# Optimization experiments

Hardware: AMD Instinct MI355X
Metric: run time of the kernel (lower is better)

Reference implementation:

```python
import jax, jax.numpy as jnp
import numpy as np

D_MODEL = 1024
N_HEADS = 16
D_K = D_MODEL // N_HEADS
BATCH = 2
SEQ = 2048


def setup_inputs() -> dict:
    key = jax.random.key(0)
    ks = jax.random.split(key, 9)
    s = 1.0 / np.sqrt(D_MODEL)
    x = jax.random.normal(ks[0], (BATCH, SEQ, D_MODEL), dtype=jnp.float32)
    # nn.Linear params: weight [out, in], bias [out]
    w_q = jax.random.uniform(ks[1], (D_MODEL, D_MODEL), jnp.float32, -s, s)
    b_q = jax.random.uniform(ks[2], (D_MODEL,), jnp.float32, -s, s)
    w_k = jax.random.uniform(ks[3], (D_MODEL, D_MODEL), jnp.float32, -s, s)
    b_k = jax.random.uniform(ks[4], (D_MODEL,), jnp.float32, -s, s)
    w_v = jax.random.uniform(ks[5], (D_MODEL, D_MODEL), jnp.float32, -s, s)
    b_v = jax.random.uniform(ks[6], (D_MODEL,), jnp.float32, -s, s)
    w_o = jax.random.uniform(ks[7], (D_MODEL, D_MODEL), jnp.float32, -s, s)
    b_o = jax.random.uniform(ks[8], (D_MODEL,), jnp.float32, -s, s)
    return {"x": x, "w_q": w_q, "b_q": b_q, "w_k": w_k, "b_k": b_k,
            "w_v": w_v, "b_v": b_v, "w_o": w_o, "b_o": b_o}


def reference(x, w_q, b_q, w_k, b_k, w_v, b_v, w_o, b_o):
    B, S, _ = x.shape
    # Linear projections, then split heads: [B, H, S, d_k]
    def proj(w, b):
        y = jnp.einsum('bsd,ed->bse', x, w) + b
        return y.reshape(B, S, N_HEADS, D_K).transpose(0, 2, 1, 3)
    q = proj(w_q, b_q)
    k = proj(w_k, b_k)
    v = proj(w_v, b_v)
    scores = jnp.einsum('bhqd,bhkd->bhqk', q, k) / jnp.sqrt(jnp.float32(D_K))
    attn = jax.nn.softmax(scores, axis=-1)  # dropout is identity in eval mode
    out = jnp.einsum('bhqk,bhkd->bhqd', attn, v)
    out = out.transpose(0, 2, 1, 3).reshape(B, S, D_MODEL)
    out = jnp.einsum('bsd,ed->bse', out, w_o) + b_o
    return out, attn
```

## Files before the change

### kernel.cpp

```cpp
#include <hip/hip_runtime.h>
#include <hip/hip_bf16.h>
#include <stdint.h>


typedef __attribute__((ext_vector_type(4))) float f32x4;
typedef __attribute__((ext_vector_type(8))) short s16x8;
typedef __attribute__((ext_vector_type(4))) unsigned int u32x4;
typedef __attribute__((ext_vector_type(4))) unsigned short u16x4;

#define MFMA(a, b, c) __builtin_amdgcn_mfma_f32_16x16x32_bf16((a), (b), (c), 0, 0, 0)

#if __has_builtin(__builtin_amdgcn_exp2f)
#define EXP2(x) __builtin_amdgcn_exp2f(x)
#else
#define EXP2(x) exp2f(x)
#endif

__device__ __forceinline__ unsigned short f2bf(float f) {
    unsigned int u = __float_as_uint(f);
    unsigned int r = (u + 0x7FFFu + ((u >> 16) & 1u)) >> 16;
    return (unsigned short)r;
}
__device__ __forceinline__ unsigned int cvtpk_bf16(float lo, float hi) {
    unsigned int r;
    asm("v_cvt_pk_bf16_f32 %0, %1, %2" : "=v"(r) : "v"(lo), "v"(hi));
    return r;
}

__global__ void convert_kernel(const float* __restrict__ x,
                               const float* __restrict__ wq, const float* __restrict__ wk,
                               const float* __restrict__ wv, const float* __restrict__ wo,
                               unsigned short* __restrict__ xb, unsigned short* __restrict__ wb) {
    size_t g = (size_t)blockIdx.x * blockDim.x + threadIdx.x;
    size_t i4 = g * 4;
    const float* src;
    unsigned short* dst;
    size_t off;
    if (i4 < 4194304) {
        src = x; dst = xb; off = i4;
    } else {
        size_t j = i4 - 4194304;
        int wsel = (int)(j >> 20);
        off = j & 1048575;
        src = (wsel == 0) ? wq : (wsel == 1) ? wk : (wsel == 2) ? wv : wo;
        dst = wb + ((size_t)wsel << 20);
    }
    float4 v = *(const float4*)(src + off);
    u16x4 o;
    o[0] = f2bf(v.x); o[1] = f2bf(v.y); o[2] = f2bf(v.z); o[3] = f2bf(v.w);
    *(u16x4*)(dst + off) = o;
}

__global__ __launch_bounds__(256, 3) void gemm_kernel(
    const unsigned short* __restrict__ A, const unsigned short* __restrict__ B,
    const float* __restrict__ bias_q, const float* __restrict__ bias_k,
    const float* __restrict__ bias_v, int mode,
    unsigned short* __restrict__ Qs, unsigned short* __restrict__ Kb,
    unsigned short* __restrict__ Vt, float* __restrict__ outp) {
    const int t = threadIdx.x;
    const int lane = t & 63;
    const int wv4 = t >> 6;
    const int wr = wv4 >> 1, wc = wv4 & 1;
    const int rowbase = blockIdx.y * 128;
    const int colbase = blockIdx.x * 128;

    __shared__ __align__(16) unsigned short lA[128 * 64];
    __shared__ __align__(16) unsigned short lB[128 * 64];

    const int crow = lane >> 3;
    const int ccol = (lane & 7) * 8;

    f32x4 acc[4][4];
#pragma unroll
    for (int mi = 0; mi < 4; ++mi)
#pragma unroll
        for (int ni = 0; ni < 4; ++ni)
            acc[mi][ni] = (f32x4){0.f, 0.f, 0.f, 0.f};

    const int l15 = lane & 15;
    const int koff = (lane >> 4) * 8;
    const int ar = wr * 64 + l15;
    const int br = wc * 64 + l15;

    for (int kt = 0; kt < 16; ++kt) {
        const int kbase = kt * 64 + ccol;
#pragma unroll
        for (int i = 0; i < 4; ++i) {
            const int c = wv4 * 4 + i;
            const int r = c * 8 + crow;
            __builtin_amdgcn_global_load_lds(
                (const __attribute__((address_space(1))) void*)(A + (size_t)(rowbase + r) * 1024 + kbase),
                (__attribute__((address_space(3))) void*)&lA[c * 512], 16, 0, 0);
            __builtin_amdgcn_global_load_lds(
                (const __attribute__((address_space(1))) void*)(B + (size_t)(colbase + r) * 1024 + kbase),
                (__attribute__((address_space(3))) void*)&lB[c * 512], 16, 0, 0);
        }
        __syncthreads();
#pragma unroll
        for (int kk = 0; kk < 2; ++kk) {
            s16x8 af[4], bf[4];
#pragma unroll
            for (int mi = 0; mi < 4; ++mi)
                af[mi] = *(const s16x8*)&lA[(ar + mi * 16) * 64 + kk * 32 + koff];
#pragma unroll
            for (int ni = 0; ni < 4; ++ni)
                bf[ni] = *(const s16x8*)&lB[(br + ni * 16) * 64 + kk * 32 + koff];
#pragma unroll
            for (int mi = 0; mi < 4; ++mi)
#pragma unroll
                for (int ni = 0; ni < 4; ++ni)
                    acc[mi][ni] = MFMA(af[mi], bf[ni], acc[mi][ni]);
        }
        __syncthreads();
    }

    if (mode == 1) {
#pragma unroll
        for (int ni = 0; ni < 4; ++ni) {
            int n = colbase + wc * 64 + ni * 16 + l15;
            float bv = bias_q[n];
#pragma unroll
            for (int mi = 0; mi < 4; ++mi) {
#pragma unroll
                for (int reg = 0; reg < 4; ++reg) {
                    int m = rowbase + wr * 64 + mi * 16 + (lane >> 4) * 4 + reg;
                    outp[(size_t)m * 1024 + n] = acc[mi][ni][reg] + bv;
                }
            }
        }
    } else {
        const int proj = colbase >> 10;
        const float* bias = (proj == 0) ? bias_q : (proj == 1) ? bias_k : bias_v;
        const float scale = (proj == 0) ? 0.18033688011112042f : 1.0f;
#pragma unroll
        for (int ni = 0; ni < 4; ++ni) {
            int n = colbase + wc * 64 + ni * 16 + l15;
            int nn = n & 1023;
            int h = nn >> 6, d = nn & 63;
            float bv = bias[nn];
#pragma unroll
            for (int mi = 0; mi < 4; ++mi) {
                int m0 = rowbase + wr * 64 + mi * 16 + (lane >> 4) * 4;
                int b = m0 >> 11, s0 = m0 & 2047;
                if (proj == 2) {
                    u16x4 pk;
#pragma unroll
                    for (int reg = 0; reg < 4; ++reg)
                        pk[reg] = f2bf(acc[mi][ni][reg] + bv);
                    int j0 = s0 & 31;
                    int pg = (j0 >> 2) & 3, pn = (j0 >> 4) & 1;
                    int pcol = (s0 & ~31) | (pg << 3) | (pn << 2);
                    *(u16x4*)&Vt[((size_t)(b * 16 + h) * 64 + d) * 2048 + pcol] = pk;
                } else {
                    unsigned short* dstp = (proj == 0) ? Qs : Kb;
#pragma unroll
                    for (int reg = 0; reg < 4; ++reg)
                        dstp[((size_t)(b * 16 + h) * 2048 + (s0 + reg)) * 64 + d] =
                            f2bf((acc[mi][ni][reg] + bv) * scale);
                }
            }
        }
    }
}

__global__ __launch_bounds__(256, 2) void attn_kernel(
    const unsigned short* __restrict__ Qs, const unsigned short* __restrict__ Kb,
    const unsigned short* __restrict__ Vt, float* __restrict__ attn,
    unsigned short* __restrict__ ctx) {
    const int t = threadIdx.x;
    const int lane = t & 63;
    const int l15 = lane & 15;
    const int g = lane >> 4;
    const int g4 = g * 4, g8 = g * 8;
    const int w = t >> 6;
    const int wr = w >> 1, wc = w & 1;
    const int qt = blockIdx.x;
    const int bh = blockIdx.y;
    const int b = bh >> 4, h = bh & 15;

    const unsigned short* Qh = Qs + (size_t)bh * (2048 * 64);
    const unsigned short* Kh = Kb + (size_t)bh * (2048 * 64);
    const unsigned short* Vh = Vt + (size_t)bh * (64 * 2048);
    float* attn_h = attn + (size_t)bh * (2048 * 2048) + (size_t)(qt * 128) * 2048;

    __shared__ float lred[2][128];
    __shared__ float lO[2][64 * 65];

    s16x8 qf[8];
#pragma unroll
    for (int mi = 0; mi < 4; ++mi)
#pragma unroll
        for (int kk = 0; kk < 2; ++kk)
            qf[mi * 2 + kk] =
                *(const s16x8*)&Qh[(size_t)(qt * 128 + wr * 64 + mi * 16 + l15) * 64 + kk * 32 + g8];

    s16x8 kf0[4], kf1[4], vf0[4], vf1[4];

#define K_LOAD(DST, KT)                                                                     \
    {                                                                                       \
        _Pragma("unroll") for (int ni = 0; ni < 2; ++ni)                                    \
            _Pragma("unroll") for (int kk = 0; kk < 2; ++kk)                                \
                DST[ni * 2 + kk] = *(const s16x8*)&Kh[(size_t)((KT) * 64 + wc * 32 +        \
                                                               ni * 16 + l15) * 64 +        \
                                                      kk * 32 + g8];                        \
    }
#define V_LOAD(DST, KT)                                                                     \
    {                                                                                       \
        _Pragma("unroll") for (int db = 0; db < 4; ++db)                                    \
            DST[db] = *(const s16x8*)&Vh[(size_t)(db * 16 + l15) * 2048 +                   \
                                         (KT) * 64 + wc * 32 + g8];                         \
    }
#define QK_MFMA(KF, SACC)                                                                   \
    {                                                                                       \
        _Pragma("unroll") for (int kk = 0; kk < 2; ++kk)                                    \
            _Pragma("unroll") for (int mi = 0; mi < 4; ++mi)                                \
                _Pragma("unroll") for (int ni = 0; ni < 2; ++ni)                            \
                    SACC[mi][ni] = MFMA(KF[ni * 2 + kk], qf[mi * 2 + kk], SACC[mi][ni]);    \
    }

    float qsum[4] = {0.f, 0.f, 0.f, 0.f};
    K_LOAD(kf0, 0);
#define P1_BODY(KF, KFN, KT)                                                                \
    {                                                                                       \
        f32x4 sacc[4][2];                                                                   \
        _Pragma("unroll") for (int mi = 0; mi < 4; ++mi)                                    \
            _Pragma("unroll") for (int ni = 0; ni < 2; ++ni)                                \
                sacc[mi][ni] = (f32x4){0.f, 0.f, 0.f, 0.f};                                 \
        QK_MFMA(KF, sacc);                                                                  \
        if ((KT) < 31) K_LOAD(KFN, (KT) + 1);                                               \
        _Pragma("unroll") for (int mi = 0; mi < 4; ++mi) {                                  \
            float e = 0.f;                                                                  \
            _Pragma("unroll") for (int ni = 0; ni < 2; ++ni)                                \
                _Pragma("unroll") for (int r = 0; r < 4; ++r)                               \
                    e += EXP2(sacc[mi][ni][r]);                                             \
            qsum[mi] += e;                                                                  \
        }                                                                                   \
    }
    for (int k2 = 0; k2 < 16; ++k2) {
        P1_BODY(kf0, kf1, 2 * k2);
        P1_BODY(kf1, kf0, 2 * k2 + 1);
    }
#pragma unroll
    for (int mi = 0; mi < 4; ++mi) {
        float v = qsum[mi];
        v += __shfl_xor(v, 16);
        v += __shfl_xor(v, 32);
        qsum[mi] = v;
    }
    if (lane < 16) {
#pragma unroll
        for (int mi = 0; mi < 4; ++mi)
            lred[wc][wr * 64 + mi * 16 + lane] = qsum[mi];
    }
    __syncthreads();
    float rl[4];
#pragma unroll
    for (int mi = 0; mi < 4; ++mi) {
        int q = wr * 64 + mi * 16 + l15;
        rl[mi] = 1.0f / (lred[0][q] + lred[1][q]);
    }

    f32x4 oacc[4][4];
#pragma unroll
    for (int mi = 0; mi < 4; ++mi)
#pragma unroll
        for (int db = 0; db < 4; ++db) oacc[mi][db] = (f32x4){0.f, 0.f, 0.f, 0.f};

    K_LOAD(kf0, 0);
    V_LOAD(vf0, 0);
#define P2_BODY(KF, KFN, VF, VFN, KT)                                                       \
    {                                                                                       \
        f32x4 sacc[4][2];                                                                   \
        _Pragma("unroll") for (int mi = 0; mi < 4; ++mi)                                    \
            _Pragma("unroll") for (int ni = 0; ni < 2; ++ni)                                \
                sacc[mi][ni] = (f32x4){0.f, 0.f, 0.f, 0.f};                                 \
        QK_MFMA(KF, sacc);                                                                  \
        if ((KT) < 31) {                                                                    \
            K_LOAD(KFN, (KT) + 1);                                                          \
            V_LOAD(VFN, (KT) + 1);                                                          \
        }                                                                                   \
        s16x8 pf[4];                                                                        \
        _Pragma("unroll") for (int mi = 0; mi < 4; ++mi) {                                  \
            const int q = wr * 64 + mi * 16 + l15;                                          \
            float p[8];                                                                     \
            _Pragma("unroll") for (int ni = 0; ni < 2; ++ni) {                              \
                p[ni * 4 + 0] = EXP2(sacc[mi][ni][0]) * rl[mi];                             \
                p[ni * 4 + 1] = EXP2(sacc[mi][ni][1]) * rl[mi];                             \
                p[ni * 4 + 2] = EXP2(sacc[mi][ni][2]) * rl[mi];                             \
                p[ni * 4 + 3] = EXP2(sacc[mi][ni][3]) * rl[mi];                             \
                float4 pv = {p[ni * 4 + 0], p[ni * 4 + 1], p[ni * 4 + 2], p[ni * 4 + 3]};   \
                *(float4*)&attn_h[(size_t)q * 2048 + (KT) * 64 + wc * 32 + ni * 16 + g4] =  \
                    pv;                                                                     \
            }                                                                               \
            u32x4 pkw;                                                                      \
            pkw[0] = cvtpk_bf16(p[0], p[1]);                                                \
            pkw[1] = cvtpk_bf16(p[2], p[3]);                                                \
            pkw[2] = cvtpk_bf16(p[4], p[5]);                                                \
            pkw[3] = cvtpk_bf16(p[6], p[7]);                                                \
            pf[mi] = *(const s16x8*)&pkw;                                                   \
        }                                                                                   \
        _Pragma("unroll") for (int mi = 0; mi < 4; ++mi)                                    \
            _Pragma("unroll") for (int db = 0; db < 4; ++db)                                \
                oacc[mi][db] = MFMA(pf[mi], VF[db], oacc[mi][db]);                          \
    }
    for (int k2 = 0; k2 < 16; ++k2) {
        P2_BODY(kf0, kf1, vf0, vf1, 2 * k2);
        P2_BODY(kf1, kf0, vf1, vf0, 2 * k2 + 1);
    }

    if (wc == 1) {
#pragma unroll
        for (int mi = 0; mi < 4; ++mi)
#pragma unroll
            for (int db = 0; db < 4; ++db)
#pragma unroll
                for (int r = 0; r < 4; ++r)
                    lO[wr][(mi * 16 + g4 + r) * 65 + db * 16 + l15] = oacc[mi][db][r];
    }
    __syncthreads();
    if (wc == 0) {
#pragma unroll
        for (int mi = 0; mi < 4; ++mi) {
#pragma unroll
            for (int db = 0; db < 4; ++db) {
#pragma unroll
                for (int r = 0; r < 4; ++r) {
                    float s = oacc[mi][db][r] + lO[wr][(mi * 16 + g4 + r) * 65 + db * 16 + l15];
                    int q = qt * 128 + wr * 64 + mi * 16 + g4 + r;
                    ctx[((size_t)(b * 2048 + q)) * 1024 + h * 64 + db * 16 + l15] = f2bf(s);
                }
            }
        }
    }
#undef K_LOAD
#undef V_LOAD
#undef QK_MFMA
#undef P1_BODY
#undef P2_BODY
}

extern "C" void kernel_launch(void* const* d_in, const int* in_sizes, int n_in,
                              void* d_out, int out_size, void* d_ws, size_t ws_size,
                              hipStream_t stream) {
    const float* x  = (const float*)d_in[0];
    const float* wq = (const float*)d_in[1];
    const float* bq = (const float*)d_in[2];
    const float* wk = (const float*)d_in[3];
    const float* bk = (const float*)d_in[4];
    const float* wv = (const float*)d_in[5];
    const float* bv = (const float*)d_in[6];
    const float* wo = (const float*)d_in[7];
    const float* bo = (const float*)d_in[8];

    char* ws = (char*)d_ws;
    unsigned short* xb  = (unsigned short*)(ws);
    unsigned short* wb  = (unsigned short*)(ws + 8388608);
    unsigned short* Qsc = (unsigned short*)(ws + 16777216);
    unsigned short* Kb  = (unsigned short*)(ws + 25165824);
    unsigned short* Vt  = (unsigned short*)(ws + 33554432);
    unsigned short* ctx = (unsigned short*)(ws + 41943040);

    float* out  = (float*)d_out;
    float* attn = out + 4194304;

    convert_kernel<<<8192, 256, 0, stream>>>(x, wq, wk, wv, wo, xb, wb);
    gemm_kernel<<<dim3(24, 32), 256, 0, stream>>>(xb, wb, bq, bk, bv, 0,
                                                  Qsc, Kb, Vt, nullptr);
    attn_kernel<<<dim3(16, 32), 256, 0, stream>>>(Qsc, Kb, Vt, attn, ctx);
    gemm_kernel<<<dim3(8, 32), 256, 0, stream>>>(ctx, wb + 3 * 1048576, bo, bo, bo, 1,
                                                 nullptr, nullptr, nullptr, out);
}
```

Before: 276.6 us.

## Restructure attention kernel to one 16-row query strip per wave, 512 threads

The attention kernel now uses 512-thread blocks where each of 8 waves owns 16 query rows across all 64 key columns of a tile. This removes the cross-wave LDS reductions for the softmax denominator and the output accumulator, along with both __syncthreads. A swizzled 1D block index spreads work across XCDs. The explicit double-buffered K/V register prefetch is dropped in favour of plain loads inside each iteration. Each wave now reloads the full K/V tiles, so per-block global/L2 traffic rises and latency hiding depends on occupancy.

```diff
diff --git a/kernel.cpp b/kernel.cpp
--- a/kernel.cpp
+++ b/kernel.cpp
@@ -6,6 +6,7 @@
 typedef __attribute__((ext_vector_type(4))) float f32x4;
 typedef __attribute__((ext_vector_type(8))) short s16x8;
 typedef __attribute__((ext_vector_type(4))) unsigned int u32x4;
+typedef __attribute__((ext_vector_type(2))) unsigned int u32x2;
 typedef __attribute__((ext_vector_type(4))) unsigned short u16x4;
 
 #define MFMA(a, b, c) __builtin_amdgcn_mfma_f32_16x16x32_bf16((a), (b), (c), 0, 0, 0)
@@ -163,7 +164,7 @@
     }
 }
 
-__global__ __launch_bounds__(256, 2) void attn_kernel(
+__global__ __launch_bounds__(512, 4) void attn_kernel(
     const unsigned short* __restrict__ Qs, const unsigned short* __restrict__ Kb,
     const unsigned short* __restrict__ Vt, float* __restrict__ attn,
     unsigned short* __restrict__ ctx) {
@@ -173,170 +174,113 @@
     const int g = lane >> 4;
     const int g4 = g * 4, g8 = g * 8;
     const int w = t >> 6;
-    const int wr = w >> 1, wc = w & 1;
-    const int qt = blockIdx.x;
-    const int bh = blockIdx.y;
+
+    const int wid = (blockIdx.x & 7) * 64 + (blockIdx.x >> 3);
+    const int bh = wid >> 4;
+    const int qt = wid & 15;
     const int b = bh >> 4, h = bh & 15;
 
     const unsigned short* Qh = Qs + (size_t)bh * (2048 * 64);
     const unsigned short* Kh = Kb + (size_t)bh * (2048 * 64);
     const unsigned short* Vh = Vt + (size_t)bh * (64 * 2048);
-    float* attn_h = attn + (size_t)bh * (2048 * 2048) + (size_t)(qt * 128) * 2048;
-
-    __shared__ float lred[2][128];
-    __shared__ float lO[2][64 * 65];
-
-    s16x8 qf[8];
-#pragma unroll
-    for (int mi = 0; mi < 4; ++mi)
+    float* attn_h = attn + (size_t)bh * (2048 * 2048);
+
+    const int qrow = qt * 128 + w * 16;
+
+    s16x8 qf[2];
+#pragma unroll
+    for (int kk = 0; kk < 2; ++kk)
+        qf[kk] = *(const s16x8*)&Qh[(size_t)(qrow + l15) * 64 + kk * 32 + g8];
+
+    float qsum = 0.f;
+    for (int kt = 0; kt < 32; ++kt) {
+        s16x8 kf[8];
+#pragma unroll
+        for (int ni = 0; ni < 4; ++ni)
+#pragma unroll
+            for (int kk = 0; kk < 2; ++kk)
+                kf[ni * 2 + kk] =
+                    *(const s16x8*)&Kh[(size_t)(kt * 64 + ni * 16 + l15) * 64 + kk * 32 + g8];
+        f32x4 sacc[4];
+#pragma unroll
+        for (int ni = 0; ni < 4; ++ni) sacc[ni] = (f32x4){0.f, 0.f, 0.f, 0.f};
 #pragma unroll
         for (int kk = 0; kk < 2; ++kk)
-            qf[mi * 2 + kk] =
-                *(const s16x8*)&Qh[(size_t)(qt * 128 + wr * 64 + mi * 16 + l15) * 64 + kk * 32 + g8];
-
-    s16x8 kf0[4], kf1[4], vf0[4], vf1[4];
-
-#define K_LOAD(DST, KT)                                                                     \
-    {                                                                                       \
-        _Pragma("unroll") for (int ni = 0; ni < 2; ++ni)                                    \
-            _Pragma("unroll") for (int kk = 0; kk < 2; ++kk)                                \
-                DST[ni * 2 + kk] = *(const s16x8*)&Kh[(size_t)((KT) * 64 + wc * 32 +        \
-                                                               ni * 16 + l15) * 64 +        \
-                                                      kk * 32 + g8];                        \
-    }
-#define V_LOAD(DST, KT)                                                                     \
-    {                                                                                       \
-        _Pragma("unroll") for (int db = 0; db < 4; ++db)                                    \
-            DST[db] = *(const s16x8*)&Vh[(size_t)(db * 16 + l15) * 2048 +                   \
-                                         (KT) * 64 + wc * 32 + g8];                         \
-    }
-#define QK_MFMA(KF, SACC)                                                                   \
-    {                                                                                       \
-        _Pragma("unroll") for (int kk = 0; kk < 2; ++kk)                                    \
-            _Pragma("unroll") for (int mi = 0; mi < 4; ++mi)                                \
-                _Pragma("unroll") for (int ni = 0; ni < 2; ++ni)                            \
-                    SACC[mi][ni] = MFMA(KF[ni * 2 + kk], qf[mi * 2 + kk], SACC[mi][ni]);    \
-    }
-
-    float qsum[4] = {0.f, 0.f, 0.f, 0.f};
-    K_LOAD(kf0, 0);
-#define P1_BODY(KF, KFN, KT)                                                                \
-    {                                                                                       \
-        f32x4 sacc[4][2];                                                                   \
-        _Pragma("unroll") for (int mi = 0; mi < 4; ++mi)                                    \
-            _Pragma("unroll") for (int ni = 0; ni < 2; ++ni)                                \
-                sacc[mi][ni] = (f32x4){0.f, 0.f, 0.f, 0.f};                                 \
-        QK_MFMA(KF, sacc);                                                                  \
-        if ((KT) < 31) K_LOAD(KFN, (KT) + 1);                                               \
-        _Pragma("unroll") for (int mi = 0; mi < 4; ++mi) {                                  \
-            float e = 0.f;                                                                  \
-            _Pragma("unroll") for (int ni = 0; ni < 2; ++ni)                                \
-                _Pragma("unroll") for (int r = 0; r < 4; ++r)                               \
-                    e += EXP2(sacc[mi][ni][r]);                                             \
-            qsum[mi] += e;                                                                  \
-        }                                                                                   \
-    }
-    for (int k2 = 0; k2 < 16; ++k2) {
-        P1_BODY(kf0, kf1, 2 * k2);
-        P1_BODY(kf1, kf0, 2 * k2 + 1);
-    }
-#pragma unroll
-    for (int mi = 0; mi < 4; ++mi) {
-        float v = qsum[mi];
-        v += __shfl_xor(v, 16);
-        v += __shfl_xor(v, 32);
-        qsum[mi] = v;
-    }
-    if (lane < 16) {
-#pragma unroll
-        for (int mi = 0; mi < 4; ++mi)
-            lred[wc][wr * 64 + mi * 16 + lane] = qsum[mi];
-    }
-    __syncthreads();
-    float rl[4];
-#pragma unroll
-    for (int mi = 0; mi < 4; ++mi) {
-        int q = wr * 64 + mi * 16 + l15;
-        rl[mi] = 1.0f / (lred[0][q] + lred[1][q]);
-    }
-
-    f32x4 oacc[4][4];
-#pragma unroll
-    for (int mi = 0; mi < 4; ++mi)
-#pragma unroll
-        for (int db = 0; db < 4; ++db) oacc[mi][db] = (f32x4){0.f, 0.f, 0.f, 0.f};
-
-    K_LOAD(kf0, 0);
-    V_LOAD(vf0, 0);
-#define P2_BODY(KF, KFN, VF, VFN, KT)                                                       \
-    {                                                                                       \
-        f32x4 sacc[4][2];                                                                   \
-        _Pragma("unroll") for (int mi = 0; mi < 4; ++mi)                                    \
-            _Pragma("unroll") for (int ni = 0; ni < 2; ++ni)                                \
-                sacc[mi][ni] = (f32x4){0.f, 0.f, 0.f, 0.f};                                 \
-        QK_MFMA(KF, sacc);                                                                  \
-        if ((KT) < 31) {                                                                    \
-            K_LOAD(KFN, (KT) + 1);                                                          \
-            V_LOAD(VFN, (KT) + 1);                                                          \
-        }                                                                                   \
-        s16x8 pf[4];                                                                        \
-        _Pragma("unroll") for (int mi = 0; mi < 4; ++mi) {                                  \
-            const int q = wr * 64 + mi * 16 + l15;                                          \
-            float p[8];                                                                     \
-            _Pragma("unroll") for (int ni = 0; ni < 2; ++ni) {                              \
-                p[ni * 4 + 0] = EXP2(sacc[mi][ni][0]) * rl[mi];                             \
-                p[ni * 4 + 1] = EXP2(sacc[mi][ni][1]) * rl[mi];                             \
-                p[ni * 4 + 2] = EXP2(sacc[mi][ni][2]) * rl[mi];                             \
-                p[ni * 4 + 3] = EXP2(sacc[mi][ni][3]) * rl[mi];                             \
-                float4 pv = {p[ni * 4 + 0], p[ni * 4 + 1], p[ni * 4 + 2], p[ni * 4 + 3]};   \
-                *(float4*)&attn_h[(size_t)q * 2048 + (KT) * 64 + wc * 32 + ni * 16 + g4] =  \
-                    pv;                                                                     \
-            }                                                                               \
-            u32x4 pkw;                                                                      \
-            pkw[0] = cvtpk_bf16(p[0], p[1]);                                                \
-            pkw[1] = cvtpk_bf16(p[2], p[3]);                                                \
-            pkw[2] = cvtpk_bf16(p[4], p[5]);                                                \
-            pkw[3] = cvtpk_bf16(p[6], p[7]);                                                \
-            pf[mi] = *(const s16x8*)&pkw;                                                   \
-        }                                                                                   \
-        _Pragma("unroll") for (int mi = 0; mi < 4; ++mi)                                    \
-            _Pragma("unroll") for (int db = 0; db < 4; ++db)                                \
-                oacc[mi][db] = MFMA(pf[mi], VF[db], oacc[mi][db]);                          \
-    }
-    for (int k2 = 0; k2 < 16; ++k2) {
-        P2_BODY(kf0, kf1, vf0, vf1, 2 * k2);
-        P2_BODY(kf1, kf0, vf1, vf0, 2 * k2 + 1);
-    }
-
-    if (wc == 1) {
-#pragma unroll
-        for (int mi = 0; mi < 4; ++mi)
-#pragma unroll
-            for (int db = 0; db < 4; ++db)
-#pragma unroll
-                for (int r = 0; r < 4; ++r)
-                    lO[wr][(mi * 16 + g4 + r) * 65 + db * 16 + l15] = oacc[mi][db][r];
-    }
-    __syncthreads();
-    if (wc == 0) {
-#pragma unroll
-        for (int mi = 0; mi < 4; ++mi) {
-#pragma unroll
-            for (int db = 0; db < 4; ++db) {
-#pragma unroll
-                for (int r = 0; r < 4; ++r) {
-                    float s = oacc[mi][db][r] + lO[wr][(mi * 16 + g4 + r) * 65 + db * 16 + l15];
-                    int q = qt * 128 + wr * 64 + mi * 16 + g4 + r;
-                    ctx[((size_t)(b * 2048 + q)) * 1024 + h * 64 + db * 16 + l15] = f2bf(s);
-                }
+#pragma unroll
+            for (int ni = 0; ni < 4; ++ni)
+                sacc[ni] = MFMA(kf[ni * 2 + kk], qf[kk], sacc[ni]);
+#pragma unroll
+        for (int ni = 0; ni < 4; ++ni)
+#pragma unroll
+            for (int r = 0; r < 4; ++r) qsum += EXP2(sacc[ni][r]);
+    }
+    qsum += __shfl_xor(qsum, 16);
+    qsum += __shfl_xor(qsum, 32);
+    const float rl = 1.0f / qsum;
+
+    f32x4 oacc[4];
+#pragma unroll
+    for (int db = 0; db < 4; ++db) oacc[db] = (f32x4){0.f, 0.f, 0.f, 0.f};
+
+    for (int kt = 0; kt < 32; ++kt) {
+        s16x8 kf[8];
+#pragma unroll
+        for (int ni = 0; ni < 4; ++ni)
+#pragma unroll
+            for (int kk = 0; kk < 2; ++kk)
+                kf[ni * 2 + kk] =
+                    *(const s16x8*)&Kh[(size_t)(kt * 64 + ni * 16 + l15) * 64 + kk * 32 + g8];
+        s16x8 vf[8];
+#pragma unroll
+        for (int db = 0; db < 4; ++db)
+#pragma unroll
+            for (int ks = 0; ks < 2; ++ks)
+                vf[db * 2 + ks] =
+                    *(const s16x8*)&Vh[(size_t)(db * 16 + l15) * 2048 + kt * 64 + ks * 32 + g8];
+        f32x4 sacc[4];
+#pragma unroll
+        for (int ni = 0; ni < 4; ++ni) sacc[ni] = (f32x4){0.f, 0.f, 0.f, 0.f};
+#pragma unroll
+        for (int kk = 0; kk < 2; ++kk)
+#pragma unroll
+            for (int ni = 0; ni < 4; ++ni)
+                sacc[ni] = MFMA(kf[ni * 2 + kk], qf[kk], sacc[ni]);
+
+        s16x8 pf[2];
+        const int q = qrow + l15;
+#pragma unroll
+        for (int ks = 0; ks < 2; ++ks) {
+            u32x2 w0, w1;
+#pragma unroll
+            for (int nn = 0; nn < 2; ++nn) {
+                const int ni = ks * 2 + nn;
+                float p0 = EXP2(sacc[ni][0]) * rl;
+                float p1 = EXP2(sacc[ni][1]) * rl;
+                float p2 = EXP2(sacc[ni][2]) * rl;
+                float p3 = EXP2(sacc[ni][3]) * rl;
+                f32x4 pv = {p0, p1, p2, p3};
+                *(f32x4*)&attn_h[(size_t)q * 2048 + kt * 64 + ni * 16 + g4] = pv;
+                if (nn == 0) { w0[0] = cvtpk_bf16(p0, p1); w0[1] = cvtpk_bf16(p2, p3); }
+                else         { w1[0] = cvtpk_bf16(p0, p1); w1[1] = cvtpk_bf16(p2, p3); }
             }
-        }
-    }
-#undef K_LOAD
-#undef V_LOAD
-#undef QK_MFMA
-#undef P1_BODY
-#undef P2_BODY
+            u32x4 pkw = {w0[0], w0[1], w1[0], w1[1]};
+            pf[ks] = *(const s16x8*)&pkw;
+        }
+#pragma unroll
+        for (int db = 0; db < 4; ++db) {
+            oacc[db] = MFMA(pf[0], vf[db * 2 + 0], oacc[db]);
+            oacc[db] = MFMA(pf[1], vf[db * 2 + 1], oacc[db]);
+        }
+    }
+
+#pragma unroll
+    for (int db = 0; db < 4; ++db) {
+#pragma unroll
+        for (int r = 0; r < 4; ++r) {
+            int q = qrow + g4 + r;
+            ctx[((size_t)(b * 2048 + q)) * 1024 + h * 64 + db * 16 + l15] = f2bf(oacc[db][r]);
+        }
+    }
 }
 
 extern "C" void kernel_launch(void* const* d_in, const int* in_sizes, int n_in,
@@ -366,7 +310,7 @@
     convert_kernel<<<8192, 256, 0, stream>>>(x, wq, wk, wv, wo, xb, wb);
     gemm_kernel<<<dim3(24, 32), 256, 0, stream>>>(xb, wb, bq, bk, bv, 0,
                                                   Qsc, Kb, Vt, nullptr);
-    attn_kernel<<<dim3(16, 32), 256, 0, stream>>>(Qsc, Kb, Vt, attn, ctx);
+    attn_kernel<<<512, 512, 0, stream>>>(Qsc, Kb, Vt, attn, ctx);
     gemm_kernel<<<dim3(8, 32), 256, 0, stream>>>(ctx, wb + 3 * 1048576, bo, bo, bo, 1,
                                                  nullptr, nullptr, nullptr, out);
 }
```

New measurement: 468.6 us. 69.4% more time.
